# Kernel tuning notes

Hardware: AMD Instinct MI355X
Metric: run time of the kernel (lower is better)

## Reference

```python
import jax, jax.numpy as jnp
import numpy as np

HEAD_SIZE = 32


def setup_inputs() -> dict:
    key = jax.random.key(0)
    ks = jax.random.split(key, 9)
    B, N, M = 2, 512, 512
    Dq = Dk = Dv = 128
    De = 64
    H, O, OUT = 8, HEAD_SIZE, 128
    s = 0.05  # keep logits tame
    return {
        "query": jax.random.normal(ks[0], (B, N, Dq), jnp.float32),
        "key": jax.random.normal(ks[1], (B, M, Dk), jnp.float32),
        "value": jax.random.normal(ks[2], (B, M, Dv), jnp.float32),
        "edge": jax.random.normal(ks[3], (B, N, M, De), jnp.float32),
        "query_kernel": jax.random.normal(ks[4], (H, Dq, O), jnp.float32) * s,
        "key_kernel": jax.random.normal(ks[5], (H, Dk + De, O), jnp.float32) * s,
        "value_kernel": jax.random.normal(ks[6], (H, Dv, O), jnp.float32) * s,
        "projection_kernel": jax.random.normal(ks[7], (H, O, OUT), jnp.float32) * s,
        "projection_bias": jnp.zeros((OUT,), jnp.float32),
    }


def reference(query, key, value, edge, query_kernel, key_kernel,
              value_kernel, projection_kernel, projection_bias):
    # Edge-conditioned keys: concat broadcast key [B,1,M,Dk] with edge [B,N,M,De]
    B, N, _ = query.shape
    M = key.shape[-2]
    key_rep = jnp.broadcast_to(key[..., None, :, :], (B, N, M, key.shape[-1]))
    key_cat = jnp.concatenate([key_rep, edge], axis=-1)           # [B,N,M,Dk+De]
    k = jnp.einsum('bnmi,hio->bnmho', key_cat, key_kernel)        # [B,N,M,H,O]
    q = jnp.einsum('bni,hio->bnho', query, query_kernel)
    q = q / jnp.sqrt(jnp.asarray(HEAD_SIZE, q.dtype))
    v = jnp.einsum('bmi,hio->bmho', value, value_kernel)
    logits = jnp.einsum('bnho,bnmho->bhnm', q, k)                 # [B,H,N,M]
    attn = jax.nn.softmax(logits, axis=-1)
    mh = jnp.einsum('bhnm,bmho->bnho', attn, v)                   # [B,N,H,O]
    out = jnp.einsum('bnhi,hio->bno', mh, projection_kernel)
    out = out + projection_bias
    return out
```

## Files before the change

### kernel.cpp

```cpp
#include <hip/hip_runtime.h>
#include <hip/hip_bf16.h>

#define B_   2
#define N_   512
#define M_   512
#define D_   128
#define DE_  64
#define H_   8
#define O_   32
#define OUT_ 128
#define DKE_ 192
#define MP_  516
#define BTP_ 200

typedef unsigned short u16;
typedef unsigned int   u32;
typedef short bf16x8 __attribute__((ext_vector_type(8)));
typedef float floatx4 __attribute__((ext_vector_type(4)));

__device__ __forceinline__ u32 pk2bf(float a, float b) {
    __hip_bfloat162 h = __float22bfloat162_rn(make_float2(a, b));
    return *reinterpret_cast<u32*>(&h);
}
__device__ __forceinline__ u16 f2bf(float a) {
    __hip_bfloat16 h = __float2bfloat16(a);
    return *reinterpret_cast<u16*>(&h);
}

__global__ __launch_bounds__(256) void k_proj_a(
    const float* __restrict__ query, const float* __restrict__ Wq,
    const float* __restrict__ Wk, u16* __restrict__ qE)
{
    const int r0 = blockIdx.x * 8;
    const int t  = threadIdx.x;
    __shared__ float Xs[8][D_];
    __shared__ float qh[8][H_ * O_];

    reinterpret_cast<float4*>(&Xs[0][0])[t] =
        reinterpret_cast<const float4*>(query + (size_t)r0 * D_)[t];
    __syncthreads();

    {
        float acc[8] = {0,0,0,0,0,0,0,0};
        const float* wcol = Wq + (t >> 5) * (D_ * O_) + (t & 31);
        for (int k = 0; k < D_; k += 4) {
            const float w0 = wcol[(k+0) * O_];
            const float w1 = wcol[(k+1) * O_];
            const float w2 = wcol[(k+2) * O_];
            const float w3 = wcol[(k+3) * O_];
#pragma unroll
            for (int r = 0; r < 8; ++r) {
                const float4 x = *reinterpret_cast<const float4*>(&Xs[r][k]);
                acc[r] += x.x * w0 + x.y * w1 + x.z * w2 + x.w * w3;
            }
        }
#pragma unroll
        for (int r = 0; r < 8; ++r) qh[r][t] = acc[r] * 0.17677669529663687f;
    }
    __syncthreads();

    for (int s = 0; s < 6; ++s) {
        const int hj = t + 256 * s;
        const int h  = hj / DKE_;
        float w[O_];
#pragma unroll
        for (int i = 0; i < O_ / 4; ++i) {
            const float4 x = reinterpret_cast<const float4*>(Wk + (size_t)hj * O_)[i];
            w[4*i] = x.x; w[4*i+1] = x.y; w[4*i+2] = x.z; w[4*i+3] = x.w;
        }
#pragma unroll
        for (int r = 0; r < 8; ++r) {
            const float* qrow = &qh[r][h * O_];
            float a = 0.f;
#pragma unroll
            for (int i = 0; i < O_ / 4; ++i) {
                const float4 qx = *reinterpret_cast<const float4*>(qrow + 4*i);
                a += qx.x * w[4*i] + qx.y * w[4*i+1] + qx.z * w[4*i+2] + qx.w * w[4*i+3];
            }
            qE[(size_t)(r0 + r) * (H_ * DKE_) + hj] = f2bf(a);
        }
    }
}

__global__ __launch_bounds__(256) void k_proj_v(
    const float* __restrict__ value, const float* __restrict__ Wv,
    float* __restrict__ vo)
{
    const int r0 = blockIdx.x * 8;
    const int t  = threadIdx.x;
    __shared__ float Xs[8][D_];
    reinterpret_cast<float4*>(&Xs[0][0])[t] =
        reinterpret_cast<const float4*>(value + (size_t)r0 * D_)[t];
    __syncthreads();

    float acc[8] = {0,0,0,0,0,0,0,0};
    const float* wcol = Wv + (t >> 5) * (D_ * O_) + (t & 31);
    for (int k = 0; k < D_; k += 4) {
        const float w0 = wcol[(k+0) * O_];
        const float w1 = wcol[(k+1) * O_];
        const float w2 = wcol[(k+2) * O_];
        const float w3 = wcol[(k+3) * O_];
#pragma unroll
        for (int r = 0; r < 8; ++r) {
            const float4 x = *reinterpret_cast<const float4*>(&Xs[r][k]);
            acc[r] += x.x * w0 + x.y * w1 + x.z * w2 + x.w * w3;
        }
    }
#pragma unroll
    for (int r = 0; r < 8; ++r) vo[(size_t)(r0 + r) * (H_ * O_) + t] = acc[r];
}

__global__ __launch_bounds__(256, 3) void k_attn(
    const float* __restrict__ key, const float* __restrict__ edge,
    const u16* __restrict__ qE, const float* __restrict__ vv,
    const float* __restrict__ Wp, const float* __restrict__ bias,
    float* __restrict__ out)
{
    const int idx  = blockIdx.x;
    const int b    = idx >> 9;
    const int t    = threadIdx.x;
    const int lane = t & 63;
    const int wv   = t >> 6;

    __shared__ __attribute__((aligned(16))) u16 Bt[4][16][BTP_];
    __shared__ __attribute__((aligned(16))) float attn_s[H_][MP_];
    __shared__ float mh_s[H_ * O_];
    __shared__ float part_s[2][OUT_];

    bf16x8 afr[6];
    {
        const int ar = lane & 15, aq = lane >> 4;
        if (ar < 8) {
            const u16* ab = qE + (size_t)idx * (H_ * DKE_) + ar * DKE_;
#pragma unroll
            for (int kk = 0; kk < 6; ++kk)
                afr[kk] = *reinterpret_cast<const bf16x8*>(ab + kk * 32 + aq * 8);
        } else {
#pragma unroll
            for (int kk = 0; kk < 6; ++kk) afr[kk] = bf16x8{0,0,0,0,0,0,0,0};
        }
    }

    const float* keyb = key  + (size_t)b   * M_ * D_;
    const float* eb   = edge + (size_t)idx * M_ * DE_;
    const int r  = lane >> 2;
    const int s4 = lane & 3;

    float4 kreg[2][8], ereg[2][4];

    {
        const int m0 = wv * 16;
        const float* kr = keyb + (size_t)(m0 + r) * D_ + s4 * 32;
        const float* er = eb   + (size_t)(m0 + r) * DE_ + s4 * 16;
#pragma unroll
        for (int i = 0; i < 8; ++i) kreg[0][i] = *reinterpret_cast<const float4*>(kr + i * 4);
#pragma unroll
        for (int i = 0; i < 4; ++i) ereg[0][i] = *reinterpret_cast<const float4*>(er + i * 4);
    }

    int buf = 0;
    for (int it = 0; it < 8; ++it) {
        const int tl = it * 4 + wv;
        if (it < 7) {
            const int m0 = (tl + 4) * 16;
            const float* kr = keyb + (size_t)(m0 + r) * D_ + s4 * 32;
            const float* er = eb   + (size_t)(m0 + r) * DE_ + s4 * 16;
#pragma unroll
            for (int i = 0; i < 8; ++i) kreg[buf^1][i] = *reinterpret_cast<const float4*>(kr + i * 4);
#pragma unroll
            for (int i = 0; i < 4; ++i) ereg[buf^1][i] = *reinterpret_cast<const float4*>(er + i * 4);
        }
        {
            u16* dst = &Bt[wv][r][0];
#pragma unroll
            for (int i = 0; i < 8; ++i) {
                uint2 p;
                p.x = pk2bf(kreg[buf][i].x, kreg[buf][i].y);
                p.y = pk2bf(kreg[buf][i].z, kreg[buf][i].w);
                *reinterpret_cast<uint2*>(dst + s4 * 32 + i * 4) = p;
            }
#pragma unroll
            for (int i = 0; i < 4; ++i) {
                uint2 p;
                p.x = pk2bf(ereg[buf][i].x, ereg[buf][i].y);
                p.y = pk2bf(ereg[buf][i].z, ereg[buf][i].w);
                *reinterpret_cast<uint2*>(dst + D_ + s4 * 16 + i * 4) = p;
            }
        }
        {
            const int br = lane & 15, q = lane >> 4;
            floatx4 acc = {0.f, 0.f, 0.f, 0.f};
#pragma unroll
            for (int kk = 0; kk < 6; ++kk) {
                const bf16x8 bfr = *reinterpret_cast<const bf16x8*>(&Bt[wv][br][kk * 32 + q * 8]);
                acc = __builtin_amdgcn_mfma_f32_16x16x32_bf16(afr[kk], bfr, acc, 0, 0, 0);
            }
            if (q < 2) {
#pragma unroll
                for (int i = 0; i < 4; ++i)
                    attn_s[q * 4 + i][tl * 16 + br] = acc[i];
            }
        }
        buf ^= 1;
    }
    __syncthreads();

    {
        const int h = t >> 5, ml = t & 31;
        float mx = -3.4e38f;
#pragma unroll 2
        for (int j = 0; j < 16; ++j) mx = fmaxf(mx, attn_s[h][ml + 32 * j]);
#pragma unroll
        for (int mask = 16; mask >= 1; mask >>= 1) mx = fmaxf(mx, __shfl_xor(mx, mask, 64));
        float sum = 0.f;
#pragma unroll 2
        for (int j = 0; j < 16; ++j) {
            const int m = ml + 32 * j;
            const float p = __expf(attn_s[h][m] - mx);
            attn_s[h][m] = p;
            sum += p;
        }
#pragma unroll
        for (int mask = 16; mask >= 1; mask >>= 1) sum += __shfl_xor(sum, mask, 64);
        const float inv = 1.f / sum;
#pragma unroll 2
        for (int j = 0; j < 16; ++j) attn_s[h][ml + 32 * j] *= inv;
    }
    __syncthreads();

    {
        const int hh = t >> 5;
        const float* vb = vv + (size_t)b * M_ * (H_ * O_) + t;
        float a0 = 0.f, a1 = 0.f, a2 = 0.f, a3 = 0.f;
        for (int m = 0; m < M_; m += 4) {
            const float4 aw = *reinterpret_cast<const float4*>(&attn_s[hh][m]);
            a0 += aw.x * vb[(size_t)(m + 0) * 256];
            a1 += aw.y * vb[(size_t)(m + 1) * 256];
            a2 += aw.z * vb[(size_t)(m + 2) * 256];
            a3 += aw.w * vb[(size_t)(m + 3) * 256];
        }
        mh_s[t] = (a0 + a1) + (a2 + a3);
    }
    __syncthreads();

    {
        const int half = t >> 7;
        const int c = t & 127;
        float acc = 0.f;
        const int j0 = half * 128;
#pragma unroll 8
        for (int jj = 0; jj < 128; ++jj)
            acc += mh_s[j0 + jj] * Wp[(size_t)(j0 + jj) * OUT_ + c];
        part_s[half][c] = acc;
    }
    __syncthreads();
    if (t < OUT_)
        out[(size_t)idx * OUT_ + t] = part_s[0][t] + part_s[1][t] + bias[t];
}

extern "C" void kernel_launch(void* const* d_in, const int* in_sizes, int n_in,
                              void* d_out, int out_size, void* d_ws, size_t ws_size,
                              hipStream_t stream)
{
    const float* query = (const float*)d_in[0];
    const float* key   = (const float*)d_in[1];
    const float* value = (const float*)d_in[2];
    const float* edge  = (const float*)d_in[3];
    const float* Wq    = (const float*)d_in[4];
    const float* Wk    = (const float*)d_in[5];
    const float* Wv    = (const float*)d_in[6];
    const float* Wp    = (const float*)d_in[7];
    const float* bias  = (const float*)d_in[8];
    float* out = (float*)d_out;

    u16*   qE_ws = (u16*)d_ws;
    float* v_ws  = (float*)((char*)d_ws + (size_t)B_*N_*H_*DKE_*2);

    k_proj_a<<<(B_ * N_) / 8, 256, 0, stream>>>(query, Wq, Wk, qE_ws);
    k_proj_v<<<(B_ * M_) / 8, 256, 0, stream>>>(value, Wv, v_ws);
    k_attn  <<<B_ * N_, 256, 0, stream>>>(key, edge, qE_ws, v_ws, Wp, bias, out);
}
```

Baseline: 289.8 us.

## Load key/edge directly into MFMA fragments, store V transposed in bf16, merge projection kernels

The attention kernel now loads key and edge rows straight into the MFMA B-fragment layout and converts them in registers. This removes the shared-memory staging buffer and the software double-buffering. The value projection is fused into one projection launch and writes V transposed in bf16, so the attn·V loop reads contiguous 16-byte vectors per thread. Occupancy is raised to 4 blocks per SM. The trade-offs are lower V precision and the loss of explicit prefetch overlap for the key/edge loads.

```diff
diff --git a/kernel.cpp b/kernel.cpp
--- a/kernel.cpp
+++ b/kernel.cpp
@@ -11,7 +11,6 @@
 #define OUT_ 128
 #define DKE_ 192
 #define MP_  516
-#define BTP_ 200
 
 typedef unsigned short u16;
 typedef unsigned int   u32;
@@ -26,23 +25,79 @@
     __hip_bfloat16 h = __float2bfloat16(a);
     return *reinterpret_cast<u16*>(&h);
 }
-
-__global__ __launch_bounds__(256) void k_proj_a(
+__device__ __forceinline__ float bf2f(u16 x) {
+    return __uint_as_float(((u32)x) << 16);
+}
+__device__ __forceinline__ bf16x8 cvt8(const float4 a, const float4 b) {
+    union { u32 u[4]; bf16x8 v; } r;
+    r.u[0] = pk2bf(a.x, a.y); r.u[1] = pk2bf(a.z, a.w);
+    r.u[2] = pk2bf(b.x, b.y); r.u[3] = pk2bf(b.z, b.w);
+    return r.v;
+}
+
+__global__ __launch_bounds__(256) void k_proj(
     const float* __restrict__ query, const float* __restrict__ Wq,
-    const float* __restrict__ Wk, u16* __restrict__ qE)
+    const float* __restrict__ Wk,
+    const float* __restrict__ value, const float* __restrict__ Wv,
+    u16* __restrict__ qE, u16* __restrict__ vvT)
 {
-    const int r0 = blockIdx.x * 8;
-    const int t  = threadIdx.x;
+    const int t = threadIdx.x;
     __shared__ float Xs[8][D_];
     __shared__ float qh[8][H_ * O_];
 
-    reinterpret_cast<float4*>(&Xs[0][0])[t] =
-        reinterpret_cast<const float4*>(query + (size_t)r0 * D_)[t];
-    __syncthreads();
-
-    {
+    if (blockIdx.x < 128) {
+        const int r0 = blockIdx.x * 8;
+        reinterpret_cast<float4*>(&Xs[0][0])[t] =
+            reinterpret_cast<const float4*>(query + (size_t)r0 * D_)[t];
+        __syncthreads();
+        {
+            float acc[8] = {0,0,0,0,0,0,0,0};
+            const float* wcol = Wq + (t >> 5) * (D_ * O_) + (t & 31);
+            for (int k = 0; k < D_; k += 4) {
+                const float w0 = wcol[(k+0) * O_];
+                const float w1 = wcol[(k+1) * O_];
+                const float w2 = wcol[(k+2) * O_];
+                const float w3 = wcol[(k+3) * O_];
+#pragma unroll
+                for (int r = 0; r < 8; ++r) {
+                    const float4 x = *reinterpret_cast<const float4*>(&Xs[r][k]);
+                    acc[r] += x.x * w0 + x.y * w1 + x.z * w2 + x.w * w3;
+                }
+            }
+#pragma unroll
+            for (int r = 0; r < 8; ++r) qh[r][t] = acc[r] * 0.17677669529663687f;
+        }
+        __syncthreads();
+
+        for (int s = 0; s < 6; ++s) {
+            const int hj = t + 256 * s;
+            const int h  = hj / DKE_;
+            float w[O_];
+#pragma unroll
+            for (int i = 0; i < O_ / 4; ++i) {
+                const float4 x = reinterpret_cast<const float4*>(Wk + (size_t)hj * O_)[i];
+                w[4*i] = x.x; w[4*i+1] = x.y; w[4*i+2] = x.z; w[4*i+3] = x.w;
+            }
+#pragma unroll
+            for (int r = 0; r < 8; ++r) {
+                const float* qrow = &qh[r][h * O_];
+                float a = 0.f;
+#pragma unroll
+                for (int i = 0; i < O_ / 4; ++i) {
+                    const float4 qx = *reinterpret_cast<const float4*>(qrow + 4*i);
+                    a += qx.x * w[4*i] + qx.y * w[4*i+1] + qx.z * w[4*i+2] + qx.w * w[4*i+3];
+                }
+                qE[(size_t)(r0 + r) * (H_ * DKE_) + hj] = f2bf(a);
+            }
+        }
+    } else {
+        const int r0 = (blockIdx.x - 128) * 8;
+        reinterpret_cast<float4*>(&Xs[0][0])[t] =
+            reinterpret_cast<const float4*>(value + (size_t)r0 * D_)[t];
+        __syncthreads();
+
         float acc[8] = {0,0,0,0,0,0,0,0};
-        const float* wcol = Wq + (t >> 5) * (D_ * O_) + (t & 31);
+        const float* wcol = Wv + (t >> 5) * (D_ * O_) + (t & 31);
         for (int k = 0; k < D_; k += 4) {
             const float w0 = wcol[(k+0) * O_];
             const float w1 = wcol[(k+1) * O_];
@@ -54,65 +109,19 @@
                 acc[r] += x.x * w0 + x.y * w1 + x.z * w2 + x.w * w3;
             }
         }
-#pragma unroll
-        for (int r = 0; r < 8; ++r) qh[r][t] = acc[r] * 0.17677669529663687f;
-    }
-    __syncthreads();
-
-    for (int s = 0; s < 6; ++s) {
-        const int hj = t + 256 * s;
-        const int h  = hj / DKE_;
-        float w[O_];
-#pragma unroll
-        for (int i = 0; i < O_ / 4; ++i) {
-            const float4 x = reinterpret_cast<const float4*>(Wk + (size_t)hj * O_)[i];
-            w[4*i] = x.x; w[4*i+1] = x.y; w[4*i+2] = x.z; w[4*i+3] = x.w;
-        }
-#pragma unroll
-        for (int r = 0; r < 8; ++r) {
-            const float* qrow = &qh[r][h * O_];
-            float a = 0.f;
-#pragma unroll
-            for (int i = 0; i < O_ / 4; ++i) {
-                const float4 qx = *reinterpret_cast<const float4*>(qrow + 4*i);
-                a += qx.x * w[4*i] + qx.y * w[4*i+1] + qx.z * w[4*i+2] + qx.w * w[4*i+3];
-            }
-            qE[(size_t)(r0 + r) * (H_ * DKE_) + hj] = f2bf(a);
-        }
-    }
-}
-
-__global__ __launch_bounds__(256) void k_proj_v(
-    const float* __restrict__ value, const float* __restrict__ Wv,
-    float* __restrict__ vo)
-{
-    const int r0 = blockIdx.x * 8;
-    const int t  = threadIdx.x;
-    __shared__ float Xs[8][D_];
-    reinterpret_cast<float4*>(&Xs[0][0])[t] =
-        reinterpret_cast<const float4*>(value + (size_t)r0 * D_)[t];
-    __syncthreads();
-
-    float acc[8] = {0,0,0,0,0,0,0,0};
-    const float* wcol = Wv + (t >> 5) * (D_ * O_) + (t & 31);
-    for (int k = 0; k < D_; k += 4) {
-        const float w0 = wcol[(k+0) * O_];
-        const float w1 = wcol[(k+1) * O_];
-        const float w2 = wcol[(k+2) * O_];
-        const float w3 = wcol[(k+3) * O_];
-#pragma unroll
-        for (int r = 0; r < 8; ++r) {
-            const float4 x = *reinterpret_cast<const float4*>(&Xs[r][k]);
-            acc[r] += x.x * w0 + x.y * w1 + x.z * w2 + x.w * w3;
-        }
-    }
-#pragma unroll
-    for (int r = 0; r < 8; ++r) vo[(size_t)(r0 + r) * (H_ * O_) + t] = acc[r];
-}
-
-__global__ __launch_bounds__(256, 3) void k_attn(
+        const int bb = r0 >> 9, m0 = r0 & 511;
+        union { u32 u[4]; uint4 q; } pk;
+        pk.u[0] = pk2bf(acc[0], acc[1]);
+        pk.u[1] = pk2bf(acc[2], acc[3]);
+        pk.u[2] = pk2bf(acc[4], acc[5]);
+        pk.u[3] = pk2bf(acc[6], acc[7]);
+        *reinterpret_cast<uint4*>(vvT + (size_t)bb * 256 * M_ + (size_t)t * M_ + m0) = pk.q;
+    }
+}
+
+__global__ __launch_bounds__(256, 4) void k_attn(
     const float* __restrict__ key, const float* __restrict__ edge,
-    const u16* __restrict__ qE, const float* __restrict__ vv,
+    const u16* __restrict__ qE, const u16* __restrict__ vvT,
     const float* __restrict__ Wp, const float* __restrict__ bias,
     float* __restrict__ out)
 {
@@ -122,86 +131,55 @@
     const int lane = t & 63;
     const int wv   = t >> 6;
 
-    __shared__ __attribute__((aligned(16))) u16 Bt[4][16][BTP_];
     __shared__ __attribute__((aligned(16))) float attn_s[H_][MP_];
     __shared__ float mh_s[H_ * O_];
     __shared__ float part_s[2][OUT_];
 
+    const int br = lane & 15;
+    const int q  = lane >> 4;
+
     bf16x8 afr[6];
-    {
-        const int ar = lane & 15, aq = lane >> 4;
-        if (ar < 8) {
-            const u16* ab = qE + (size_t)idx * (H_ * DKE_) + ar * DKE_;
-#pragma unroll
-            for (int kk = 0; kk < 6; ++kk)
-                afr[kk] = *reinterpret_cast<const bf16x8*>(ab + kk * 32 + aq * 8);
-        } else {
-#pragma unroll
-            for (int kk = 0; kk < 6; ++kk) afr[kk] = bf16x8{0,0,0,0,0,0,0,0};
-        }
+    if (br < 8) {
+        const u16* ab = qE + (size_t)idx * (H_ * DKE_) + br * DKE_;
+#pragma unroll
+        for (int kk = 0; kk < 6; ++kk)
+            afr[kk] = *reinterpret_cast<const bf16x8*>(ab + kk * 32 + q * 8);
+    } else {
+#pragma unroll
+        for (int kk = 0; kk < 6; ++kk) afr[kk] = bf16x8{0,0,0,0,0,0,0,0};
     }
 
     const float* keyb = key  + (size_t)b   * M_ * D_;
     const float* eb   = edge + (size_t)idx * M_ * DE_;
-    const int r  = lane >> 2;
-    const int s4 = lane & 3;
-
-    float4 kreg[2][8], ereg[2][4];
-
-    {
-        const int m0 = wv * 16;
-        const float* kr = keyb + (size_t)(m0 + r) * D_ + s4 * 32;
-        const float* er = eb   + (size_t)(m0 + r) * DE_ + s4 * 16;
-#pragma unroll
-        for (int i = 0; i < 8; ++i) kreg[0][i] = *reinterpret_cast<const float4*>(kr + i * 4);
-#pragma unroll
-        for (int i = 0; i < 4; ++i) ereg[0][i] = *reinterpret_cast<const float4*>(er + i * 4);
-    }
-
-    int buf = 0;
+
     for (int it = 0; it < 8; ++it) {
         const int tl = it * 4 + wv;
-        if (it < 7) {
-            const int m0 = (tl + 4) * 16;
-            const float* kr = keyb + (size_t)(m0 + r) * D_ + s4 * 32;
-            const float* er = eb   + (size_t)(m0 + r) * DE_ + s4 * 16;
-#pragma unroll
-            for (int i = 0; i < 8; ++i) kreg[buf^1][i] = *reinterpret_cast<const float4*>(kr + i * 4);
-#pragma unroll
-            for (int i = 0; i < 4; ++i) ereg[buf^1][i] = *reinterpret_cast<const float4*>(er + i * 4);
-        }
-        {
-            u16* dst = &Bt[wv][r][0];
-#pragma unroll
-            for (int i = 0; i < 8; ++i) {
-                uint2 p;
-                p.x = pk2bf(kreg[buf][i].x, kreg[buf][i].y);
-                p.y = pk2bf(kreg[buf][i].z, kreg[buf][i].w);
-                *reinterpret_cast<uint2*>(dst + s4 * 32 + i * 4) = p;
-            }
-#pragma unroll
-            for (int i = 0; i < 4; ++i) {
-                uint2 p;
-                p.x = pk2bf(ereg[buf][i].x, ereg[buf][i].y);
-                p.y = pk2bf(ereg[buf][i].z, ereg[buf][i].w);
-                *reinterpret_cast<uint2*>(dst + D_ + s4 * 16 + i * 4) = p;
-            }
-        }
-        {
-            const int br = lane & 15, q = lane >> 4;
-            floatx4 acc = {0.f, 0.f, 0.f, 0.f};
-#pragma unroll
-            for (int kk = 0; kk < 6; ++kk) {
-                const bf16x8 bfr = *reinterpret_cast<const bf16x8*>(&Bt[wv][br][kk * 32 + q * 8]);
-                acc = __builtin_amdgcn_mfma_f32_16x16x32_bf16(afr[kk], bfr, acc, 0, 0, 0);
-            }
-            if (q < 2) {
-#pragma unroll
-                for (int i = 0; i < 4; ++i)
-                    attn_s[q * 4 + i][tl * 16 + br] = acc[i];
-            }
-        }
-        buf ^= 1;
+        const int m  = tl * 16 + br;
+        const float* kr = keyb + (size_t)m * D_  + q * 8;
+        const float* er = eb   + (size_t)m * DE_ + q * 8;
+        float4 kf[8], ef[4];
+#pragma unroll
+        for (int kk = 0; kk < 4; ++kk) {
+            kf[2*kk]   = *reinterpret_cast<const float4*>(kr + kk * 32);
+            kf[2*kk+1] = *reinterpret_cast<const float4*>(kr + kk * 32 + 4);
+        }
+#pragma unroll
+        for (int kk = 0; kk < 2; ++kk) {
+            ef[2*kk]   = *reinterpret_cast<const float4*>(er + kk * 32);
+            ef[2*kk+1] = *reinterpret_cast<const float4*>(er + kk * 32 + 4);
+        }
+        floatx4 acc = {0.f, 0.f, 0.f, 0.f};
+#pragma unroll
+        for (int kk = 0; kk < 4; ++kk)
+            acc = __builtin_amdgcn_mfma_f32_16x16x32_bf16(afr[kk], cvt8(kf[2*kk], kf[2*kk+1]), acc, 0, 0, 0);
+#pragma unroll
+        for (int kk = 0; kk < 2; ++kk)
+            acc = __builtin_amdgcn_mfma_f32_16x16x32_bf16(afr[4+kk], cvt8(ef[2*kk], ef[2*kk+1]), acc, 0, 0, 0);
+        if (q < 2) {
+#pragma unroll
+            for (int i = 0; i < 4; ++i)
+                attn_s[q * 4 + i][tl * 16 + br] = acc[i];
+        }
     }
     __syncthreads();
 
@@ -230,16 +208,18 @@
 
     {
         const int hh = t >> 5;
-        const float* vb = vv + (size_t)b * M_ * (H_ * O_) + t;
-        float a0 = 0.f, a1 = 0.f, a2 = 0.f, a3 = 0.f;
-        for (int m = 0; m < M_; m += 4) {
-            const float4 aw = *reinterpret_cast<const float4*>(&attn_s[hh][m]);
-            a0 += aw.x * vb[(size_t)(m + 0) * 256];
-            a1 += aw.y * vb[(size_t)(m + 1) * 256];
-            a2 += aw.z * vb[(size_t)(m + 2) * 256];
-            a3 += aw.w * vb[(size_t)(m + 3) * 256];
-        }
-        mh_s[t] = (a0 + a1) + (a2 + a3);
+        const u16* vrow = vvT + (size_t)b * 256 * M_ + (size_t)t * M_;
+        float a0 = 0.f, a1 = 0.f;
+        for (int m0 = 0; m0 < M_; m0 += 8) {
+            const bf16x8 v8 = *reinterpret_cast<const bf16x8*>(vrow + m0);
+            const float4 w0 = *reinterpret_cast<const float4*>(&attn_s[hh][m0]);
+            const float4 w1 = *reinterpret_cast<const float4*>(&attn_s[hh][m0 + 4]);
+            a0 += w0.x * bf2f((u16)v8[0]) + w0.y * bf2f((u16)v8[1])
+                + w0.z * bf2f((u16)v8[2]) + w0.w * bf2f((u16)v8[3]);
+            a1 += w1.x * bf2f((u16)v8[4]) + w1.y * bf2f((u16)v8[5])
+                + w1.z * bf2f((u16)v8[6]) + w1.w * bf2f((u16)v8[7]);
+        }
+        mh_s[t] = a0 + a1;
     }
     __syncthreads();
 
@@ -273,10 +253,9 @@
     const float* bias  = (const float*)d_in[8];
     float* out = (float*)d_out;
 
-    u16*   qE_ws = (u16*)d_ws;
-    float* v_ws  = (float*)((char*)d_ws + (size_t)B_*N_*H_*DKE_*2);
-
-    k_proj_a<<<(B_ * N_) / 8, 256, 0, stream>>>(query, Wq, Wk, qE_ws);
-    k_proj_v<<<(B_ * M_) / 8, 256, 0, stream>>>(value, Wv, v_ws);
-    k_attn  <<<B_ * N_, 256, 0, stream>>>(key, edge, qE_ws, v_ws, Wp, bias, out);
-}
+    u16* qE_ws = (u16*)d_ws;
+    u16* vT_ws = (u16*)((char*)d_ws + (size_t)B_*N_*H_*DKE_*2);
+
+    k_proj<<<256,  256, 0, stream>>>(query, Wq, Wk, value, Wv, qE_ws, vT_ws);
+    k_attn<<<1024, 256, 0, stream>>>(key, edge, qE_ws, vT_ws, Wp, bias, out);
+}
```

After: 276.1 us. -4.7%, faster.
